# Kernel optimization log

Measured on AMD Instinct MI355X. Metric: run time of the kernel, lower is better.

Reference implementation:

```python
import jax, jax.numpy as jnp
import numpy as np


def setup_inputs() -> dict:
    key = jax.random.key(0)
    k1, k2, k3, k4 = jax.random.split(key, 4)
    B, N, F, H, C = 16, 4096, 8, 64, 256
    x = jax.random.normal(k1, (B, N, F, H), dtype=jnp.float32)
    W = jax.random.normal(k2, (H, 1), dtype=jnp.float32) / jnp.sqrt(jnp.float32(H))
    b = jax.random.normal(k3, (1,), dtype=jnp.float32) * 0.01
    segment_ids = jax.random.randint(k4, (N,), 0, C)
    return {"x": x, "W": W, "b": b, "segment_ids": segment_ids, "num_coarse": C}


def reference(x, W, b, segment_ids, num_coarse):
    # x: [B, N, F, H]; segment_ids: [N] -> coarse index; output: [B, C, F, H]
    B, N, Fdim, H = x.shape
    seg = segment_ids
    # node scores: Linear(hidden_dim, 1) on mean over feature axis -> [B, N]
    scores = (jnp.einsum('bnfh,ho->bn', x, W) / jnp.float32(Fdim)) + b[0]
    # numerically-stable per-segment softmax over fine nodes within each coarse group
    seg_max = jax.vmap(lambda s: jax.ops.segment_max(s, seg, num_segments=num_coarse))(scores)  # [B, C]
    e = jnp.exp(scores - seg_max[:, seg])                                                        # [B, N]
    denom = jax.vmap(lambda ee: jax.ops.segment_sum(ee, seg, num_segments=num_coarse))(e)        # [B, C]
    w = e / denom[:, seg]                                                                        # [B, N]
    # score-weighted segmented sum of fine features into coarse nodes
    pooled = jax.vmap(
        lambda wb, xb: jax.ops.segment_sum(wb[:, None, None] * xb, seg, num_segments=num_coarse)
    )(w, x)  # [B, C, F, H]
    return pooled
```

## Files before the change

kernel.cpp:

```cpp
#include <hip/hip_runtime.h>

#define B_ 16
#define N_ 4096
#define F_ 8
#define H_ 64
#define C_ 256
#define FH 512
#define CAP 256

__global__ __launch_bounds__(256) void scores_kernel(
    const float* __restrict__ x, const float* __restrict__ W,
    const float* __restrict__ bias, float* __restrict__ scores)
{
    int gtid = blockIdx.x * 256 + threadIdx.x;
    int node = gtid >> 6;
    int lane = gtid & 63;
    const float* xp = x + (size_t)node * FH;
    int f0 = lane >> 4;
    int hq = (lane & 15) * 4;
    float4 w4 = *(const float4*)(W + hq);
    float4 a  = *(const float4*)(xp + f0 * H_ + hq);
    float4 b4 = *(const float4*)(xp + (f0 + 4) * H_ + hq);
    float partial = (a.x + b4.x) * w4.x + (a.y + b4.y) * w4.y
                  + (a.z + b4.z) * w4.z + (a.w + b4.w) * w4.w;
#pragma unroll
    for (int off = 32; off > 0; off >>= 1)
        partial += __shfl_xor(partial, off, 64);
    if (lane == 0)
        scores[node] = partial * (1.0f / F_) + bias[0];
}

__device__ __forceinline__ unsigned fmap(float f) {
    unsigned u = __float_as_uint(f);
    return (u & 0x80000000u) ? ~u : (u | 0x80000000u);
}
__device__ __forceinline__ float funmap(unsigned u) {
    return (u & 0x80000000u) ? __uint_as_float(u ^ 0x80000000u)
                             : __uint_as_float(~u);
}

__global__ __launch_bounds__(256) void softmax_kernel(
    const float* __restrict__ scores, const int* __restrict__ seg,
    float* __restrict__ w)
{
    int b = blockIdx.x;
    int t = threadIdx.x;
    __shared__ unsigned smax[C_];
    __shared__ float ssum[C_];
    smax[t] = 0u;
    ssum[t] = 0.0f;
    __syncthreads();

    float sc[N_ / 256];
    int   sg[N_ / 256];
#pragma unroll
    for (int k = 0; k < N_ / 256; k++) {
        int n = t + k * 256;
        sg[k] = seg[n];
        sc[k] = scores[b * N_ + n];
        atomicMax(&smax[sg[k]], fmap(sc[k]));
    }
    __syncthreads();

    float ev[N_ / 256];
#pragma unroll
    for (int k = 0; k < N_ / 256; k++) {
        float m = funmap(smax[sg[k]]);
        ev[k] = __expf(sc[k] - m);
        atomicAdd(&ssum[sg[k]], ev[k]);
    }
    __syncthreads();

#pragma unroll
    for (int k = 0; k < N_ / 256; k++) {
        int n = t + k * 256;
        w[b * N_ + n] = ev[k] / ssum[sg[k]];
    }
}

__global__ __launch_bounds__(256) void csr_kernel(
    const int* __restrict__ seg, int* __restrict__ order,
    int* __restrict__ start)
{
    int t = threadIdx.x;
    __shared__ int cnt[C_];
    __shared__ int scan[C_];
    __shared__ int base[C_];
    cnt[t] = 0;
    __syncthreads();

    int sg[N_ / 256];
#pragma unroll
    for (int k = 0; k < N_ / 256; k++) {
        sg[k] = seg[t + k * 256];
        atomicAdd(&cnt[sg[k]], 1);
    }
    __syncthreads();

    int my = cnt[t];
    scan[t] = my;
    __syncthreads();
#pragma unroll
    for (int off = 1; off < C_; off <<= 1) {
        int v = (t >= off) ? scan[t - off] : 0;
        __syncthreads();
        scan[t] += v;
        __syncthreads();
    }
    int excl = scan[t] - my;
    start[t] = excl;
    if (t == 0) start[C_] = N_;
    base[t] = excl;
    __syncthreads();

#pragma unroll
    for (int k = 0; k < N_ / 256; k++) {
        int pos = atomicAdd(&base[sg[k]], 1);
        order[pos] = t + k * 256;
    }
}

__global__ __launch_bounds__(128) void pool_kernel(
    const float* __restrict__ x, const float* __restrict__ w,
    const int* __restrict__ order, const int* __restrict__ start,
    float* __restrict__ out)
{
    int b = blockIdx.x >> 8;
    int c = blockIdx.x & (C_ - 1);
    int t = threadIdx.x;

    int s0 = start[c];
    int m  = start[c + 1] - s0;
    if (m > CAP) m = CAP;

    __shared__ int   ln[CAP];
    __shared__ float lw[CAP];
    for (int i = t; i < m; i += 128) {
        int n = order[s0 + i];
        ln[i] = n;
        lw[i] = w[b * N_ + n];
    }
    __syncthreads();

    const float4* x4 = (const float4*)x;
    float4 acc0 = {0, 0, 0, 0}, acc1 = {0, 0, 0, 0};
    float4 acc2 = {0, 0, 0, 0}, acc3 = {0, 0, 0, 0};

    int i = 0;
    for (; i + 4 <= m; i += 4) {
        int n0 = ln[i], n1 = ln[i + 1], n2 = ln[i + 2], n3 = ln[i + 3];
        float w0 = lw[i], w1 = lw[i + 1], w2 = lw[i + 2], w3 = lw[i + 3];
        float4 v0 = x4[((size_t)(b * N_ + n0)) * (FH / 4) + t];
        float4 v1 = x4[((size_t)(b * N_ + n1)) * (FH / 4) + t];
        float4 v2 = x4[((size_t)(b * N_ + n2)) * (FH / 4) + t];
        float4 v3 = x4[((size_t)(b * N_ + n3)) * (FH / 4) + t];
        acc0.x += w0 * v0.x; acc0.y += w0 * v0.y; acc0.z += w0 * v0.z; acc0.w += w0 * v0.w;
        acc1.x += w1 * v1.x; acc1.y += w1 * v1.y; acc1.z += w1 * v1.z; acc1.w += w1 * v1.w;
        acc2.x += w2 * v2.x; acc2.y += w2 * v2.y; acc2.z += w2 * v2.z; acc2.w += w2 * v2.w;
        acc3.x += w3 * v3.x; acc3.y += w3 * v3.y; acc3.z += w3 * v3.z; acc3.w += w3 * v3.w;
    }
    for (; i < m; i++) {
        int n0 = ln[i];
        float w0 = lw[i];
        float4 v0 = x4[((size_t)(b * N_ + n0)) * (FH / 4) + t];
        acc0.x += w0 * v0.x; acc0.y += w0 * v0.y; acc0.z += w0 * v0.z; acc0.w += w0 * v0.w;
    }

    float4 r;
    r.x = (acc0.x + acc1.x) + (acc2.x + acc3.x);
    r.y = (acc0.y + acc1.y) + (acc2.y + acc3.y);
    r.z = (acc0.z + acc1.z) + (acc2.z + acc3.z);
    r.w = (acc0.w + acc1.w) + (acc2.w + acc3.w);
    ((float4*)out)[((size_t)(b * C_ + c)) * (FH / 4) + t] = r;
}

extern "C" void kernel_launch(void* const* d_in, const int* in_sizes, int n_in,
                              void* d_out, int out_size, void* d_ws, size_t ws_size,
                              hipStream_t stream)
{
    const float* x    = (const float*)d_in[0];
    const float* W    = (const float*)d_in[1];
    const float* bias = (const float*)d_in[2];
    const int*   seg  = (const int*)d_in[3];
    float* out = (float*)d_out;

    float* scores = (float*)d_ws;
    float* w      = scores + B_ * N_;
    int*   order  = (int*)(w + B_ * N_);
    int*   start  = order + N_;

    scores_kernel<<<B_ * N_ / 4, 256, 0, stream>>>(x, W, bias, scores);
    csr_kernel<<<1, 256, 0, stream>>>(seg, order, start);
    softmax_kernel<<<B_, 256, 0, stream>>>(scores, seg, w);
    pool_kernel<<<B_ * C_, 128, 0, stream>>>(x, w, order, start, out);
}
```

Baseline: 238.0 us.

## Fuse scoring, CSR build and softmax denominator; normalize inside pool kernel

Folds the CSR construction into an extra block of the score kernel. The separate softmax kernel is replaced by computing exp(score) directly and accumulating per-segment denominators with global atomics. The pool kernel then scales its weighted sum by the reciprocal denominator. This removes two launches, including the serial single-block CSR and 16-block softmax kernels, and one intermediate pass. The cost is a memset, heavy global atomic contention, and dropping the max subtraction, so large scores can overflow exp.

Result: faster. 224.1 us (-5.8%).

```diff
diff --git a/kernel.cpp b/kernel.cpp
--- a/kernel.cpp
+++ b/kernel.cpp
@@ -8,10 +8,52 @@
 #define FH 512
 #define CAP 256
 
-__global__ __launch_bounds__(256) void scores_kernel(
+__global__ __launch_bounds__(256) void score_csr_kernel(
     const float* __restrict__ x, const float* __restrict__ W,
-    const float* __restrict__ bias, float* __restrict__ scores)
+    const float* __restrict__ bias, const int* __restrict__ seg,
+    float* __restrict__ ebuf, float* __restrict__ denom,
+    int* __restrict__ order, int* __restrict__ start)
 {
+    if (blockIdx.x == B_ * N_ / 4) {
+        int t = threadIdx.x;
+        __shared__ int cnt[C_];
+        __shared__ int scan[C_];
+        __shared__ int base[C_];
+        cnt[t] = 0;
+        __syncthreads();
+
+        int sg[N_ / 256];
+#pragma unroll
+        for (int k = 0; k < N_ / 256; k++) {
+            sg[k] = seg[t + k * 256];
+            atomicAdd(&cnt[sg[k]], 1);
+        }
+        __syncthreads();
+
+        int my = cnt[t];
+        scan[t] = my;
+        __syncthreads();
+#pragma unroll
+        for (int off = 1; off < C_; off <<= 1) {
+            int v = (t >= off) ? scan[t - off] : 0;
+            __syncthreads();
+            scan[t] += v;
+            __syncthreads();
+        }
+        int excl = scan[t] - my;
+        start[t] = excl;
+        if (t == 0) start[C_] = N_;
+        base[t] = excl;
+        __syncthreads();
+
+#pragma unroll
+        for (int k = 0; k < N_ / 256; k++) {
+            int pos = atomicAdd(&base[sg[k]], 1);
+            order[pos] = t + k * 256;
+        }
+        return;
+    }
+
     int gtid = blockIdx.x * 256 + threadIdx.x;
     int node = gtid >> 6;
     int lane = gtid & 63;
@@ -26,102 +68,19 @@
 #pragma unroll
     for (int off = 32; off > 0; off >>= 1)
         partial += __shfl_xor(partial, off, 64);
-    if (lane == 0)
-        scores[node] = partial * (1.0f / F_) + bias[0];
-}
-
-__device__ __forceinline__ unsigned fmap(float f) {
-    unsigned u = __float_as_uint(f);
-    return (u & 0x80000000u) ? ~u : (u | 0x80000000u);
-}
-__device__ __forceinline__ float funmap(unsigned u) {
-    return (u & 0x80000000u) ? __uint_as_float(u ^ 0x80000000u)
-                             : __uint_as_float(~u);
-}
-
-__global__ __launch_bounds__(256) void softmax_kernel(
-    const float* __restrict__ scores, const int* __restrict__ seg,
-    float* __restrict__ w)
-{
-    int b = blockIdx.x;
-    int t = threadIdx.x;
-    __shared__ unsigned smax[C_];
-    __shared__ float ssum[C_];
-    smax[t] = 0u;
-    ssum[t] = 0.0f;
-    __syncthreads();
-
-    float sc[N_ / 256];
-    int   sg[N_ / 256];
-#pragma unroll
-    for (int k = 0; k < N_ / 256; k++) {
-        int n = t + k * 256;
-        sg[k] = seg[n];
-        sc[k] = scores[b * N_ + n];
-        atomicMax(&smax[sg[k]], fmap(sc[k]));
-    }
-    __syncthreads();
-
-    float ev[N_ / 256];
-#pragma unroll
-    for (int k = 0; k < N_ / 256; k++) {
-        float m = funmap(smax[sg[k]]);
-        ev[k] = __expf(sc[k] - m);
-        atomicAdd(&ssum[sg[k]], ev[k]);
-    }
-    __syncthreads();
-
-#pragma unroll
-    for (int k = 0; k < N_ / 256; k++) {
-        int n = t + k * 256;
-        w[b * N_ + n] = ev[k] / ssum[sg[k]];
-    }
-}
-
-__global__ __launch_bounds__(256) void csr_kernel(
-    const int* __restrict__ seg, int* __restrict__ order,
-    int* __restrict__ start)
-{
-    int t = threadIdx.x;
-    __shared__ int cnt[C_];
-    __shared__ int scan[C_];
-    __shared__ int base[C_];
-    cnt[t] = 0;
-    __syncthreads();
-
-    int sg[N_ / 256];
-#pragma unroll
-    for (int k = 0; k < N_ / 256; k++) {
-        sg[k] = seg[t + k * 256];
-        atomicAdd(&cnt[sg[k]], 1);
-    }
-    __syncthreads();
-
-    int my = cnt[t];
-    scan[t] = my;
-    __syncthreads();
-#pragma unroll
-    for (int off = 1; off < C_; off <<= 1) {
-        int v = (t >= off) ? scan[t - off] : 0;
-        __syncthreads();
-        scan[t] += v;
-        __syncthreads();
-    }
-    int excl = scan[t] - my;
-    start[t] = excl;
-    if (t == 0) start[C_] = N_;
-    base[t] = excl;
-    __syncthreads();
-
-#pragma unroll
-    for (int k = 0; k < N_ / 256; k++) {
-        int pos = atomicAdd(&base[sg[k]], 1);
-        order[pos] = t + k * 256;
+    if (lane == 0) {
+        float score = partial * (1.0f / F_) + bias[0];
+        float e = __expf(score);
+        int b = node >> 12;
+        int n = node & (N_ - 1);
+        ebuf[node] = e;
+        atomicAdd(&denom[b * C_ + seg[n]], e);
     }
 }
 
 __global__ __launch_bounds__(128) void pool_kernel(
-    const float* __restrict__ x, const float* __restrict__ w,
+    const float* __restrict__ x, const float* __restrict__ ebuf,
+    const float* __restrict__ denom,
     const int* __restrict__ order, const int* __restrict__ start,
     float* __restrict__ out)
 {
@@ -138,9 +97,12 @@
     for (int i = t; i < m; i += 128) {
         int n = order[s0 + i];
         ln[i] = n;
-        lw[i] = w[b * N_ + n];
+        lw[i] = ebuf[b * N_ + n];
     }
     __syncthreads();
+
+    float d   = denom[b * C_ + c];
+    float inv = (m > 0) ? 1.0f / d : 0.0f;
 
     const float4* x4 = (const float4*)x;
     float4 acc0 = {0, 0, 0, 0}, acc1 = {0, 0, 0, 0};
@@ -167,10 +129,10 @@
     }
 
     float4 r;
-    r.x = (acc0.x + acc1.x) + (acc2.x + acc3.x);
-    r.y = (acc0.y + acc1.y) + (acc2.y + acc3.y);
-    r.z = (acc0.z + acc1.z) + (acc2.z + acc3.z);
-    r.w = (acc0.w + acc1.w) + (acc2.w + acc3.w);
+    r.x = ((acc0.x + acc1.x) + (acc2.x + acc3.x)) * inv;
+    r.y = ((acc0.y + acc1.y) + (acc2.y + acc3.y)) * inv;
+    r.z = ((acc0.z + acc1.z) + (acc2.z + acc3.z)) * inv;
+    r.w = ((acc0.w + acc1.w) + (acc2.w + acc3.w)) * inv;
     ((float4*)out)[((size_t)(b * C_ + c)) * (FH / 4) + t] = r;
 }
 
@@ -184,13 +146,13 @@
     const int*   seg  = (const int*)d_in[3];
     float* out = (float*)d_out;
 
-    float* scores = (float*)d_ws;
-    float* w      = scores + B_ * N_;
-    int*   order  = (int*)(w + B_ * N_);
-    int*   start  = order + N_;
+    float* ebuf  = (float*)d_ws;
+    float* denom = ebuf + B_ * N_;
+    int*   order = (int*)(denom + B_ * C_);
+    int*   start = order + N_;
 
-    scores_kernel<<<B_ * N_ / 4, 256, 0, stream>>>(x, W, bias, scores);
-    csr_kernel<<<1, 256, 0, stream>>>(seg, order, start);
-    softmax_kernel<<<B_, 256, 0, stream>>>(scores, seg, w);
-    pool_kernel<<<B_ * C_, 128, 0, stream>>>(x, w, order, start, out);
+    hipMemsetAsync(denom, 0, B_ * C_ * sizeof(float), stream);
+    score_csr_kernel<<<B_ * N_ / 4 + 1, 256, 0, stream>>>(
+        x, W, bias, seg, ebuf, denom, order, start);
+    pool_kernel<<<B_ * C_, 128, 0, stream>>>(x, ebuf, denom, order, start, out);
 }
```
